# Kernel optimization log

Hardware: AMD Instinct MI355X
Metric: run time of the kernel (lower is better)

Reference implementation:

```python
import jax, jax.numpy as jnp
import numpy as np

EMBED = 384
HEAD = 64


def setup_inputs() -> dict:
    key = jax.random.key(0)
    kx, kq, kk, kv = jax.random.split(key, 4)
    B, T = 4, 4096
    x = jax.random.normal(kx, (B, T, EMBED), dtype=jnp.float32)
    # torch Linear(384, 64, bias=False): weight (64, 384), y = x @ W.T.
    # Store pre-transposed as (EMBED, HEAD) so y = x @ W.
    s = 1.0 / np.sqrt(EMBED)  # kaiming-uniform-ish scale
    Wq = jax.random.uniform(kq, (EMBED, HEAD), jnp.float32, -s, s)
    Wk = jax.random.uniform(kk, (EMBED, HEAD), jnp.float32, -s, s)
    Wv = jax.random.uniform(kv, (EMBED, HEAD), jnp.float32, -s, s)
    return {"x": x, "Wq": Wq, "Wk": Wk, "Wv": Wv}


def reference(x, Wq, Wk, Wv):
    # q, k, v: [B, T, H]
    q = x @ Wq
    k = x @ Wk
    v = x @ Wv
    scale = k.shape[-1] ** (-0.5)
    scores = jnp.einsum("bth,bsh->bts", q, k) * scale  # [B, T, T]
    # Faithful to the original: tril, then mask anything equal to 0 with -inf
    # (this also masks exact zeros inside the causal region).
    tril = jnp.tril(scores)
    masked = jnp.where(tril == 0, -jnp.inf, tril)
    attn = jax.nn.softmax(masked, axis=-1)
    out = jnp.einsum("bts,bsh->bth", attn, v)  # [B, T, H]
    return out
```

## Files before the change

kernel.cpp:

```cpp
#include <hip/hip_runtime.h>
#include <hip/hip_bf16.h>
#include <stdint.h>


#define EMBED 384
#define HEAD  64
#define NB    4
#define NT    4096
#define NROWS (NB * NT)
#define NSPLIT 4

#define SCALE_Q 0.18033688011112042f

typedef short bf16x8 __attribute__((ext_vector_type(8)));
typedef float f32x4  __attribute__((ext_vector_type(4)));

__device__ __forceinline__ unsigned short bfround(float f) {
    union { float f; unsigned u; } v; v.f = f;
    return (unsigned short)((v.u + 0x8000u) >> 16);
}
__device__ __forceinline__ unsigned packbf(float lo, float hi) {
    union { float f; unsigned u; } a, b; a.f = lo; b.f = hi;
    return ((a.u + 0x8000u) >> 16) | ((b.u + 0x8000u) & 0xFFFF0000u);
}

__device__ __forceinline__ void pl_swap32(unsigned& a, unsigned& b) {
    asm("v_permlane32_swap_b32 %0, %1" : "+v"(a), "+v"(b));
}
__device__ __forceinline__ void pl_swap16(unsigned& a, unsigned& b) {
    asm("v_permlane16_swap_b32 %0, %1" : "+v"(a), "+v"(b));
}

__global__ __launch_bounds__(256)
void wprep_kernel(const float* __restrict__ Wq,
                  const float* __restrict__ Wk,
                  const float* __restrict__ Wv,
                  unsigned short* __restrict__ Wt)
{
    int idx = blockIdx.x * 256 + threadIdx.x;
    int k = idx / 192;
    int n = idx - k * 192;
    int sel = n >> 6, nc = n & 63;
    const float* wp = (sel == 0) ? Wq : ((sel == 1) ? Wk : Wv);
    Wt[n * EMBED + k] = bfround(wp[(size_t)k * HEAD + nc]);
}

__global__ __launch_bounds__(256)
void proj_kernel(const float* __restrict__ x,
                 const unsigned short* __restrict__ Wt,
                 unsigned short* __restrict__ Qo,
                 unsigned short* __restrict__ Ko,
                 unsigned short* __restrict__ Vto)
{
    __shared__ __attribute__((aligned(16))) unsigned short ws[96][200];
    __shared__ __attribute__((aligned(16))) unsigned short xs[64][200];
    unsigned short (*vbuf)[72] = (unsigned short (*)[72])&xs[0][0];

    const int t    = threadIdx.x;
    const int w    = t >> 6;
    const int lane = t & 63;
    const int quad = lane >> 4;
    const int l16  = lane & 15;
    const int half = blockIdx.x & 1;
    const int r0   = (blockIdx.x >> 1) * 64;
    const int colbase = half * 96;

    f32x4 acc[6];
#pragma unroll
    for (int i = 0; i < 6; ++i) acc[i] = (f32x4){0.f, 0.f, 0.f, 0.f};

#pragma unroll
    for (int ph = 0; ph < 2; ++ph) {
        if (ph) __syncthreads();
        const int k0 = ph * 192;
#pragma unroll
        for (int i = 0; i < 9; ++i) {
            int idx = t + i * 256;
            int row = idx / 24, c = idx - row * 24;
            *(uint4*)&ws[row][c * 8] =
                *(const uint4*)(Wt + (size_t)(colbase + row) * EMBED + k0 + c * 8);
        }
#pragma unroll
        for (int i = 0; i < 12; ++i) {
            int idx = t + i * 256;
            int row = idx / 48, c4 = idx - row * 48;
            const float4 v = *(const float4*)(x + (size_t)(r0 + row) * EMBED + k0 + c4 * 4);
            uint2 pw; pw.x = packbf(v.x, v.y); pw.y = packbf(v.z, v.w);
            *(uint2*)&xs[row][c4 * 4] = pw;
        }
        __syncthreads();
#pragma unroll
        for (int step = 0; step < 6; ++step) {
            bf16x8 a = *(const bf16x8*)&xs[w * 16 + l16][step * 32 + quad * 8];
#pragma unroll
            for (int ng = 0; ng < 6; ++ng) {
                bf16x8 b = *(const bf16x8*)&ws[ng * 16 + l16][step * 32 + quad * 8];
                acc[ng] = __builtin_amdgcn_mfma_f32_16x16x32_bf16(a, b, acc[ng], 0, 0, 0);
            }
        }
    }
    __syncthreads();

#pragma unroll
    for (int ng = 0; ng < 6; ++ng) {
        int cg = colbase + ng * 16 + l16;
#pragma unroll
        for (int r = 0; r < 4; ++r) {
            int row = r0 + w * 16 + quad * 4 + r;
            float vv = acc[ng][r];
            if (cg < 64) {
                Qo[(size_t)row * HEAD + cg] = bfround(vv * SCALE_Q);
            } else if (cg < 128) {
                Ko[(size_t)row * HEAD + (cg - 64)] = bfround(vv);
            } else {
                vbuf[cg - 128][w * 16 + quad * 4 + r] = bfround(vv);
            }
        }
    }
    __syncthreads();
    if (half == 1) {
        const int batch = r0 >> 12;
        const int s0 = r0 & (NT - 1);
#pragma unroll
        for (int i = 0; i < 2; ++i) {
            int idx = t + i * 256;
            int d = idx >> 3, c = idx & 7;
            *(uint4*)(Vto + ((size_t)(batch * HEAD + d)) * NT + s0 + c * 8) =
                *(const uint4*)&vbuf[d][c * 8];
        }
    }
}

__global__ __launch_bounds__(256, 4)
void attn_kernel(const unsigned short* __restrict__ Qi,
                 const unsigned short* __restrict__ Ki,
                 const unsigned short* __restrict__ Vti,
                 float* __restrict__ opart,
                 float* __restrict__ lpart)
{
    __shared__ __attribute__((aligned(16))) unsigned short Kt[2][64][64];
    __shared__ __attribute__((aligned(16))) unsigned short Vs[2][64][64];

    const int t    = threadIdx.x;
    const int w    = t >> 6;
    const int lane = t & 63;
    const int quad = lane >> 4;
    const int l16  = lane & 15;

    const int u = blockIdx.x;
    const int g = u >> 4;
    const int m = (g < 32) ? (63 - g) : (g - 32);
    const int sp = (u >> 2) & 3;
    const int batch = u & 3;
    const int ntiles = (m >= sp) ? (((m - sp) >> 2) + 1) : 0;
    const int q0 = m * 64 + w * 16;

    const unsigned short* Kbg = Ki  + (size_t)batch * NT * HEAD;
    const unsigned short* Vbg = Vti + (size_t)batch * HEAD * NT;

    bf16x8 bq0, bq1;
    {
        const unsigned short* qp = Qi + (size_t)(batch * NT + q0 + l16) * HEAD + quad * 8;
        bq0 = *(const bf16x8*)(qp);
        bq1 = *(const bf16x8*)(qp + 32);
    }

    f32x4 o[4];
#pragma unroll
    for (int i = 0; i < 4; ++i) o[i] = (f32x4){0.f, 0.f, 0.f, 0.f};
    float rs = 0.f;

    const int srow0 = t >> 3, sc = t & 7;
    const int srow1 = (t + 256) >> 3;
    const int scc0 = sc ^ (srow0 & 7);
    const int scc1 = sc ^ (srow1 & 7);
    const int sw = l16 & 7;

    uint4 kr0, kr1, vr0, vr1;
    if (ntiles > 0) {
        const int kt = sp;
        kr0 = *(const uint4*)(Kbg + (size_t)(kt * 64 + srow0) * HEAD + sc * 8);
        kr1 = *(const uint4*)(Kbg + (size_t)(kt * 64 + srow1) * HEAD + sc * 8);
        vr0 = *(const uint4*)(Vbg + (size_t)srow0 * NT + kt * 64 + sc * 8);
        vr1 = *(const uint4*)(Vbg + (size_t)srow1 * NT + kt * 64 + sc * 8);
    }

    int cur = 0;
    for (int j = 0; j < ntiles; ++j) {
        const int kt = sp + 4 * j;
        *(uint4*)&Kt[cur][srow0][scc0 * 8] = kr0;
        *(uint4*)&Kt[cur][srow1][scc1 * 8] = kr1;
        *(uint4*)&Vs[cur][srow0][scc0 * 8] = vr0;
        *(uint4*)&Vs[cur][srow1][scc1 * 8] = vr1;
        __syncthreads();

        if (j + 1 < ntiles) {
            const int ktn = kt + 4;
            kr0 = *(const uint4*)(Kbg + (size_t)(ktn * 64 + srow0) * HEAD + sc * 8);
            kr1 = *(const uint4*)(Kbg + (size_t)(ktn * 64 + srow1) * HEAD + sc * 8);
            vr0 = *(const uint4*)(Vbg + (size_t)srow0 * NT + ktn * 64 + sc * 8);
            vr1 = *(const uint4*)(Vbg + (size_t)srow1 * NT + ktn * 64 + sc * 8);
        }

        const bool diag = (kt == m);
        uint2 pw[4];
#pragma unroll
        for (int ts = 0; ts < 4; ++ts) {
            bf16x8 ak0 = *(const bf16x8*)&Kt[cur][ts * 16 + l16][(quad ^ sw) * 8];
            bf16x8 ak1 = *(const bf16x8*)&Kt[cur][ts * 16 + l16][((4 + quad) ^ sw) * 8];
            f32x4 z = (f32x4){0.f, 0.f, 0.f, 0.f};
            z = __builtin_amdgcn_mfma_f32_16x16x32_bf16(ak0, bq0, z, 0, 0, 0);
            z = __builtin_amdgcn_mfma_f32_16x16x32_bf16(ak1, bq1, z, 0, 0, 0);
            float p[4];
#pragma unroll
            for (int r = 0; r < 4; ++r) {
                float pv = __builtin_amdgcn_exp2f(z[r]);
                if (diag) {
                    int sg = kt * 64 + ts * 16 + quad * 4 + r;
                    pv = (sg > q0 + l16) ? 0.f : pv;
                }
                p[r] = pv;
            }
            rs += (p[0] + p[1]) + (p[2] + p[3]);
            pw[ts].x = packbf(p[0], p[1]);
            pw[ts].y = packbf(p[2], p[3]);
        }

        unsigned a0 = pw[0].x, c0 = pw[0].y, b0 = pw[1].x, d0 = pw[1].y;
        pl_swap32(a0, b0); pl_swap32(c0, d0);
        pl_swap16(a0, b0); pl_swap16(c0, d0);
        unsigned a1 = pw[2].x, c1 = pw[2].y, b1 = pw[3].x, d1 = pw[3].y;
        pl_swap32(a1, b1); pl_swap32(c1, d1);
        pl_swap16(a1, b1); pl_swap16(c1, d1);
        union { unsigned u[4]; bf16x8 v; } ua0, ua1;
        ua0.u[0] = a0; ua0.u[1] = c0; ua0.u[2] = b0; ua0.u[3] = d0;
        ua1.u[0] = a1; ua1.u[1] = c1; ua1.u[2] = b1; ua1.u[3] = d1;
        const bf16x8 ap0 = ua0.v;
        const bf16x8 ap1 = ua1.v;

#pragma unroll
        for (int nd = 0; nd < 4; ++nd) {
            bf16x8 av0 = *(const bf16x8*)&Vs[cur][nd * 16 + l16][(quad ^ sw) * 8];
            bf16x8 av1 = *(const bf16x8*)&Vs[cur][nd * 16 + l16][((4 + quad) ^ sw) * 8];
            o[nd] = __builtin_amdgcn_mfma_f32_16x16x32_bf16(ap0, av0, o[nd], 0, 0, 0);
            o[nd] = __builtin_amdgcn_mfma_f32_16x16x32_bf16(ap1, av1, o[nd], 0, 0, 0);
        }
        cur ^= 1;
    }

    rs += __shfl_xor(rs, 16, 64);
    rs += __shfl_xor(rs, 32, 64);
    if (quad == 0)
        lpart[(size_t)sp * NROWS + batch * NT + q0 + l16] = rs;
    float* ob = opart + (size_t)sp * NROWS * HEAD;
#pragma unroll
    for (int r = 0; r < 4; ++r) {
        size_t off = (size_t)(batch * NT + q0 + quad * 4 + r) * HEAD;
#pragma unroll
        for (int nd = 0; nd < 4; ++nd)
            ob[off + nd * 16 + l16] = o[nd][r];
    }
}

__global__ __launch_bounds__(256)
void combine_kernel(const float* __restrict__ opart,
                    const float* __restrict__ lpart,
                    float* __restrict__ out)
{
    int gid = blockIdx.x * 256 + threadIdx.x;
    int row = gid >> 4;
    int d4  = (gid & 15) * 4;
    const size_t st = (size_t)NROWS * HEAD;
    const float* p0 = opart + (size_t)row * HEAD + d4;
    f32x4 a = *(const f32x4*)(p0);
    f32x4 b = *(const f32x4*)(p0 + st);
    f32x4 c = *(const f32x4*)(p0 + 2 * st);
    f32x4 d = *(const f32x4*)(p0 + 3 * st);
    float inv = 1.0f / (lpart[row] + lpart[NROWS + row] +
                        lpart[2 * NROWS + row] + lpart[3 * NROWS + row]);
    f32x4 res = (a + b) + (c + d);
    res[0] *= inv; res[1] *= inv; res[2] *= inv; res[3] *= inv;
    *(f32x4*)(out + (size_t)row * HEAD + d4) = res;
}

extern "C" void kernel_launch(void* const* d_in, const int* in_sizes, int n_in,
                              void* d_out, int out_size, void* d_ws, size_t ws_size,
                              hipStream_t stream)
{
    const float* x  = (const float*)d_in[0];
    const float* Wq = (const float*)d_in[1];
    const float* Wk = (const float*)d_in[2];
    const float* Wv = (const float*)d_in[3];
    float* out = (float*)d_out;

    unsigned short* Qw  = (unsigned short*)d_ws;
    unsigned short* Kw  = Qw + (size_t)NROWS * HEAD;
    unsigned short* Vtw = Kw + (size_t)NROWS * HEAD;
    unsigned short* Wtw = Vtw + (size_t)NROWS * HEAD;
    float* opart = (float*)(Wtw + (size_t)192 * EMBED);
    float* lpart = opart + (size_t)NSPLIT * NROWS * HEAD;

    wprep_kernel<<<(192 * EMBED) / 256, 256, 0, stream>>>(Wq, Wk, Wv, Wtw);
    proj_kernel<<<512, 256, 0, stream>>>(x, Wtw, Qw, Kw, Vtw);
    attn_kernel<<<1024, 256, 0, stream>>>(Qw, Kw, Vtw, opart, lpart);
    combine_kernel<<<NROWS * 16 / 256, 256, 0, stream>>>(opart, lpart, out);
}
```

Baseline: 106.4 us.

## Restructure projection kernel: 512-thread blocks, double-buffered K chunks, swizzled LDS

The projection kernel now uses 512-thread blocks that each compute all 192 output columns for 64 rows, instead of two blocks splitting columns. x is no longer loaded twice. K is processed in three 128-wide chunks with register prefetch and double-buffered shared memory, so global loads overlap MFMA work. An XOR swizzle replaces padding to avoid LDS bank conflicts. Fewer blocks (256) may reduce occupancy and latency hiding on a chip with many CUs.

```diff
diff --git a/kernel.cpp b/kernel.cpp
--- a/kernel.cpp
+++ b/kernel.cpp
@@ -45,89 +45,105 @@
     Wt[n * EMBED + k] = bfround(wp[(size_t)k * HEAD + nc]);
 }
 
-__global__ __launch_bounds__(256)
+__global__ __launch_bounds__(512)
 void proj_kernel(const float* __restrict__ x,
                  const unsigned short* __restrict__ Wt,
                  unsigned short* __restrict__ Qo,
                  unsigned short* __restrict__ Ko,
                  unsigned short* __restrict__ Vto)
 {
-    __shared__ __attribute__((aligned(16))) unsigned short ws[96][200];
-    __shared__ __attribute__((aligned(16))) unsigned short xs[64][200];
-    unsigned short (*vbuf)[72] = (unsigned short (*)[72])&xs[0][0];
+    __shared__ __attribute__((aligned(16))) unsigned short ws[2][192][128];
+    __shared__ __attribute__((aligned(16))) unsigned short xs[2][64][128];
+    unsigned short (*vbuf)[72] = (unsigned short (*)[72])&xs[1][0][0];
 
     const int t    = threadIdx.x;
+    const int lane = t & 63;
     const int w    = t >> 6;
-    const int lane = t & 63;
     const int quad = lane >> 4;
     const int l16  = lane & 15;
-    const int half = blockIdx.x & 1;
-    const int r0   = (blockIdx.x >> 1) * 64;
-    const int colbase = half * 96;
+    const int wr   = w & 3;
+    const int wc   = w >> 2;
+    const int r0   = blockIdx.x * 64;
+
+    const int xr  = t >> 5, xc4 = t & 31;
+    const int xch = xc4 >> 1, xsub = (xc4 & 1) * 4;
+    const int wrw = t >> 4, wcc = t & 15;
 
     f32x4 acc[6];
 #pragma unroll
     for (int i = 0; i < 6; ++i) acc[i] = (f32x4){0.f, 0.f, 0.f, 0.f};
 
-#pragma unroll
-    for (int ph = 0; ph < 2; ++ph) {
-        if (ph) __syncthreads();
-        const int k0 = ph * 192;
-#pragma unroll
-        for (int i = 0; i < 9; ++i) {
-            int idx = t + i * 256;
-            int row = idx / 24, c = idx - row * 24;
-            *(uint4*)&ws[row][c * 8] =
-                *(const uint4*)(Wt + (size_t)(colbase + row) * EMBED + k0 + c * 8);
-        }
-#pragma unroll
-        for (int i = 0; i < 12; ++i) {
-            int idx = t + i * 256;
-            int row = idx / 48, c4 = idx - row * 48;
-            const float4 v = *(const float4*)(x + (size_t)(r0 + row) * EMBED + k0 + c4 * 4);
-            uint2 pw; pw.x = packbf(v.x, v.y); pw.y = packbf(v.z, v.w);
-            *(uint2*)&xs[row][c4 * 4] = pw;
+    float4 xv[4];
+    uint4  wv[6];
+#pragma unroll
+    for (int i = 0; i < 4; ++i)
+        xv[i] = *(const float4*)(x + (size_t)(r0 + xr + 16 * i) * EMBED + xc4 * 4);
+#pragma unroll
+    for (int i = 0; i < 6; ++i)
+        wv[i] = *(const uint4*)(Wt + (size_t)(wrw + 32 * i) * EMBED + wcc * 8);
+
+    int cur = 0;
+#pragma unroll
+    for (int ph = 0; ph < 3; ++ph) {
+#pragma unroll
+        for (int i = 0; i < 4; ++i) {
+            int row = xr + 16 * i;
+            uint2 pw; pw.x = packbf(xv[i].x, xv[i].y); pw.y = packbf(xv[i].z, xv[i].w);
+            *(uint2*)&xs[cur][row][((xch ^ (row & 15)) << 3) + xsub] = pw;
+        }
+#pragma unroll
+        for (int i = 0; i < 6; ++i) {
+            int row = wrw + 32 * i;
+            *(uint4*)&ws[cur][row][(wcc ^ (row & 15)) << 3] = wv[i];
         }
         __syncthreads();
-#pragma unroll
-        for (int step = 0; step < 6; ++step) {
-            bf16x8 a = *(const bf16x8*)&xs[w * 16 + l16][step * 32 + quad * 8];
+
+        if (ph < 2) {
+            const int k0 = (ph + 1) * 128;
+#pragma unroll
+            for (int i = 0; i < 4; ++i)
+                xv[i] = *(const float4*)(x + (size_t)(r0 + xr + 16 * i) * EMBED + k0 + xc4 * 4);
+#pragma unroll
+            for (int i = 0; i < 6; ++i)
+                wv[i] = *(const uint4*)(Wt + (size_t)(wrw + 32 * i) * EMBED + k0 + wcc * 8);
+        }
+
+#pragma unroll
+        for (int s = 0; s < 4; ++s) {
+            bf16x8 a = *(const bf16x8*)&xs[cur][wr * 16 + l16][((s * 4 + quad) ^ l16) << 3];
 #pragma unroll
             for (int ng = 0; ng < 6; ++ng) {
-                bf16x8 b = *(const bf16x8*)&ws[ng * 16 + l16][step * 32 + quad * 8];
+                bf16x8 b = *(const bf16x8*)&ws[cur][wc * 96 + ng * 16 + l16][((s * 4 + quad) ^ l16) << 3];
                 acc[ng] = __builtin_amdgcn_mfma_f32_16x16x32_bf16(a, b, acc[ng], 0, 0, 0);
             }
         }
+        cur ^= 1;
     }
     __syncthreads();
 
 #pragma unroll
     for (int ng = 0; ng < 6; ++ng) {
-        int cg = colbase + ng * 16 + l16;
+        int cg = wc * 96 + ng * 16 + l16;
 #pragma unroll
         for (int r = 0; r < 4; ++r) {
-            int row = r0 + w * 16 + quad * 4 + r;
+            int row = r0 + wr * 16 + quad * 4 + r;
             float vv = acc[ng][r];
             if (cg < 64) {
                 Qo[(size_t)row * HEAD + cg] = bfround(vv * SCALE_Q);
             } else if (cg < 128) {
                 Ko[(size_t)row * HEAD + (cg - 64)] = bfround(vv);
             } else {
-                vbuf[cg - 128][w * 16 + quad * 4 + r] = bfround(vv);
+                vbuf[cg - 128][wr * 16 + quad * 4 + r] = bfround(vv);
             }
         }
     }
     __syncthreads();
-    if (half == 1) {
+    {
         const int batch = r0 >> 12;
         const int s0 = r0 & (NT - 1);
-#pragma unroll
-        for (int i = 0; i < 2; ++i) {
-            int idx = t + i * 256;
-            int d = idx >> 3, c = idx & 7;
-            *(uint4*)(Vto + ((size_t)(batch * HEAD + d)) * NT + s0 + c * 8) =
-                *(const uint4*)&vbuf[d][c * 8];
-        }
+        const int d = t >> 3, c = t & 7;
+        *(uint4*)(Vto + ((size_t)(batch * HEAD + d)) * NT + s0 + c * 8) =
+            *(const uint4*)&vbuf[d][c * 8];
     }
 }
 
@@ -301,7 +317,7 @@
     float* lpart = opart + (size_t)NSPLIT * NROWS * HEAD;
 
     wprep_kernel<<<(192 * EMBED) / 256, 256, 0, stream>>>(Wq, Wk, Wv, Wtw);
-    proj_kernel<<<512, 256, 0, stream>>>(x, Wtw, Qw, Kw, Vtw);
+    proj_kernel<<<256, 512, 0, stream>>>(x, Wtw, Qw, Kw, Vtw);
     attn_kernel<<<1024, 256, 0, stream>>>(Qw, Kw, Vtw, opart, lpart);
     combine_kernel<<<NROWS * 16 / 256, 256, 0, stream>>>(opart, lpart, out);
 }
```

Result: no change. 105.8 us (-0.6%).
